# Performance work log

Measured on AMD Instinct MI355X. Metric: run time of the kernel, lower is better.

The kernel has to match this reference:

```python
import jax, jax.numpy as jnp
import numpy as np

B, C, D, TOPK = 4096, 8192, 128, 10


def calc_distmat2(x, y):
    d = (x * x).sum(-1)[:, None] + (y * y).sum(-1)[None, :] - 2.0 * (x @ y.T)
    return jnp.clip(d, 1e-12, 1e12)


def setup_inputs() -> dict:
    key = jax.random.key(0)
    k1, k2, k3 = jax.random.split(key, 3)
    x = jax.random.normal(k1, (B, D), dtype=jnp.float32)
    labels = jax.random.randint(k2, (B,), 0, C)
    # kaiming_normal_(mode='fan_out') on (C, D): fan_out = C, gain = sqrt(2)
    centers = jax.random.normal(k3, (C, D), dtype=jnp.float32) * np.float32(np.sqrt(2.0 / C))
    return {"x": x, "labels": labels, "centers": centers, "topk": TOPK}


def reference(x, labels, centers, topk):
    num_classes = centers.shape[0]
    distmat = calc_distmat2(x, centers)                      # (B, C)
    lab = labels[:, None]                                    # (B, 1)
    dist_pull = jnp.take_along_axis(distmat, lab, axis=1)[:, 0]  # (B,)
    loss_pull = dist_pull.mean()

    # mode 'exp': per-row masked topk over negatives + log-softmax over [pos, neg_topk]
    logits = -distmat                                        # (B, C)
    pos = jnp.take_along_axis(logits, lab, axis=1)           # (B, 1)
    is_pos = lab == jnp.arange(num_classes)[None, :]         # (B, C)
    neg_logits = jnp.where(is_pos, -jnp.inf, logits)
    neg_topk, _ = jax.lax.top_k(neg_logits, topk)            # (B, topk)
    cat = jnp.concatenate([pos, neg_topk], axis=1)           # (B, 1+topk)
    # -log_softmax at index 0 (the positive) per row, averaged ('ccent')
    loss = (-jax.nn.log_softmax(cat, axis=1)[:, 0]).mean()

    # center-to-center repulsion over strictly-lower-triangular pairs
    cent2cent = calc_distmat2(centers, centers)              # (C, C)
    tri = jnp.tril(jnp.ones((num_classes, num_classes), dtype=bool), -1)
    n_pairs = num_classes * (num_classes - 1) // 2
    loss_dis = -jnp.sum(jnp.where(tri, cent2cent, 0.0)) / jnp.float32(n_pairs)

    return (loss, loss_dis, cent2cent, loss_pull)
```

## Files before the change

kernel.cpp:

```cpp
#include <hip/hip_runtime.h>
#include <hip/hip_bf16.h>
#include <math.h>

#define NB 4096
#define NC 8192
#define ND 128
#define NSPLIT 32
#define CPS (NC / NSPLIT)
#define NTILES (CPS / 16)
#define NEGINF -3.0e38f

#define WS_XN 16
#define WS_CN (WS_XN + NB)
#define WS_POS (WS_CN + NC)
#define WS_PART (WS_POS + NB)
#define WS_XB (WS_PART + NB * NSPLIT * 10)
#define WS_CB (WS_XB + NB * ND / 2)

typedef __attribute__((ext_vector_type(8))) short short8v;
typedef __attribute__((ext_vector_type(4))) float f32x4;

__global__ __launch_bounds__(256) void prep_kernel(
    const float* __restrict__ x, const float* __restrict__ c, float* __restrict__ ws) {
  if (blockIdx.x == 0 && threadIdx.x < 16) ws[threadIdx.x] = 0.0f;
  int wid = threadIdx.x >> 6, lane = threadIdx.x & 63;
  int row = blockIdx.x * 4 + wid;
  const float* src;
  float* ndst;
  ushort* bdst;
  if (row < NB) {
    src = x + (size_t)row * ND;
    ndst = ws + WS_XN + row;
    bdst = (ushort*)(ws + WS_XB) + (size_t)row * ND;
  } else {
    int r = row - NB;
    src = c + (size_t)r * ND;
    ndst = ws + WS_CN + r;
    bdst = (ushort*)(ws + WS_CB) + (size_t)r * ND;
  }
  float2 v = *(const float2*)(src + lane * 2);
  __hip_bfloat16 h0 = __float2bfloat16(v.x);
  __hip_bfloat16 h1 = __float2bfloat16(v.y);
  ushort2 u;
  u.x = *(ushort*)&h0;
  u.y = *(ushort*)&h1;
  *(ushort2*)(bdst + lane * 2) = u;
  float s = fmaf(v.x, v.x, v.y * v.y);
#pragma unroll
  for (int off = 32; off; off >>= 1) s += __shfl_down(s, off, 64);
  if (lane == 0) *ndst = s;
}

#define INS10(arr, val)                          \
  {                                              \
    float _v = (val);                            \
    _Pragma("unroll") for (int _k = 0; _k < 10; ++_k) { \
      float _mx = fmaxf(arr[_k], _v);            \
      _v = fminf(arr[_k], _v);                   \
      arr[_k] = _mx;                             \
    }                                            \
  }

#define SW(a, b) { float _x = fmaxf(a, b); b = fminf(a, b); a = _x; }

#define LOADF(d0, d1, d2, d3, IDX)                                            \
  {                                                                           \
    const ushort* cp_ = cb + (size_t)(cbase + (IDX) * 16 + lo) * ND + hi * 8; \
    d0 = *(const short8v*)(cp_ + 0);                                          \
    d1 = *(const short8v*)(cp_ + 32);                                         \
    d2 = *(const short8v*)(cp_ + 64);                                         \
    d3 = *(const short8v*)(cp_ + 96);                                         \
  }

#define EPILOGUE(TL, ACC, CN4)                                                \
  {                                                                           \
    int cb0_ = cbase + (TL) * 16 + hi * 4;                                    \
    float a0 = -(fminf(fmaxf(xn + (CN4).x - 2.0f * (ACC)[0], 1e-12f), 1e12f));\
    float a1 = -(fminf(fmaxf(xn + (CN4).y - 2.0f * (ACC)[1], 1e-12f), 1e12f));\
    float a2 = -(fminf(fmaxf(xn + (CN4).z - 2.0f * (ACC)[2], 1e-12f), 1e12f));\
    float a3 = -(fminf(fmaxf(xn + (CN4).w - 2.0f * (ACC)[3], 1e-12f), 1e12f));\
    bool l0 = (cb0_ + 0 == lab), l1 = (cb0_ + 1 == lab),                      \
         l2 = (cb0_ + 2 == lab), l3 = (cb0_ + 3 == lab);                      \
    posv = l0 ? a0 : posv; posv = l1 ? a1 : posv;                             \
    posv = l2 ? a2 : posv; posv = l3 ? a3 : posv;                             \
    a0 = l0 ? NEGINF : a0; a1 = l1 ? NEGINF : a1;                             \
    a2 = l2 ? NEGINF : a2; a3 = l3 ? NEGINF : a3;                             \
    SW(a0, a1) SW(a2, a3) SW(a0, a2) SW(a1, a3) SW(a1, a2)                    \
    float n0 = fmaxf(a0, top[0]);                                             \
    float n1 = fmaxf(fmaxf(a1, top[1]), fminf(a0, top[0]));                   \
    float n2 = fmaxf(fmaxf(a2, top[2]),                                       \
                     fmaxf(fminf(a0, top[1]), fminf(a1, top[0])));            \
    float n3 = fmaxf(fmaxf(a3, top[3]),                                       \
                     fmaxf(fmaxf(fminf(a0, top[2]), fminf(a1, top[1])),       \
                           fminf(a2, top[0])));                               \
    float n4 = fmaxf(top[4], fmaxf(fmaxf(fminf(a0, top[3]), fminf(a1, top[2])), \
                                   fmaxf(fminf(a2, top[1]), fminf(a3, top[0])))); \
    float n5 = fmaxf(top[5], fmaxf(fmaxf(fminf(a0, top[4]), fminf(a1, top[3])), \
                                   fmaxf(fminf(a2, top[2]), fminf(a3, top[1])))); \
    float n6 = fmaxf(top[6], fmaxf(fmaxf(fminf(a0, top[5]), fminf(a1, top[4])), \
                                   fmaxf(fminf(a2, top[3]), fminf(a3, top[2])))); \
    float n7 = fmaxf(top[7], fmaxf(fmaxf(fminf(a0, top[6]), fminf(a1, top[5])), \
                                   fmaxf(fminf(a2, top[4]), fminf(a3, top[3])))); \
    float n8 = fmaxf(top[8], fmaxf(fmaxf(fminf(a0, top[7]), fminf(a1, top[6])), \
                                   fmaxf(fminf(a2, top[5]), fminf(a3, top[4])))); \
    float n9 = fmaxf(top[9], fmaxf(fmaxf(fminf(a0, top[8]), fminf(a1, top[7])), \
                                   fmaxf(fminf(a2, top[6]), fminf(a3, top[5])))); \
    top[0] = n0; top[1] = n1; top[2] = n2; top[3] = n3; top[4] = n4;          \
    top[5] = n5; top[6] = n6; top[7] = n7; top[8] = n8; top[9] = n9;          \
  }

__global__ __launch_bounds__(256) void xloss_kernel(
    const int* __restrict__ labels, float* __restrict__ ws) {
  int t = threadIdx.x;
  int w = t >> 6, l = t & 63, lo = l & 15, hi = l >> 4;
  int row = blockIdx.x * 64 + w * 16 + lo;
  int cbase = blockIdx.y * CPS;

  const ushort* xb = (const ushort*)(ws + WS_XB);
  const ushort* cb = (const ushort*)(ws + WS_CB);

  const ushort* xrp = xb + (size_t)row * ND + hi * 8;
  short8v xf0 = *(const short8v*)(xrp + 0);
  short8v xf1 = *(const short8v*)(xrp + 32);
  short8v xf2 = *(const short8v*)(xrp + 64);
  short8v xf3 = *(const short8v*)(xrp + 96);

  float xn = ws[WS_XN + row];
  int lab = labels[row];

  float top[10];
#pragma unroll
  for (int k = 0; k < 10; ++k) top[k] = NEGINF;
  float posv = NEGINF;

  short8v pa0, pa1, pa2, pa3, qa0, qa1, qa2, qa3;
  f32x4 cnP, cnQ;
  LOADF(pa0, pa1, pa2, pa3, 0)
  cnP = *(const f32x4*)(ws + WS_CN + cbase + hi * 4);

  for (int tl = 0; tl < NTILES; tl += 2) {
    LOADF(qa0, qa1, qa2, qa3, tl + 1)
    cnQ = *(const f32x4*)(ws + WS_CN + cbase + (tl + 1) * 16 + hi * 4);

    f32x4 accA = {0.f, 0.f, 0.f, 0.f};
    accA = __builtin_amdgcn_mfma_f32_16x16x32_bf16(pa0, xf0, accA, 0, 0, 0);
    accA = __builtin_amdgcn_mfma_f32_16x16x32_bf16(pa1, xf1, accA, 0, 0, 0);
    accA = __builtin_amdgcn_mfma_f32_16x16x32_bf16(pa2, xf2, accA, 0, 0, 0);
    accA = __builtin_amdgcn_mfma_f32_16x16x32_bf16(pa3, xf3, accA, 0, 0, 0);
    f32x4 cnA = cnP;
    int nidx = (tl + 2 < NTILES) ? tl + 2 : tl;
    LOADF(pa0, pa1, pa2, pa3, nidx)
    cnP = *(const f32x4*)(ws + WS_CN + cbase + nidx * 16 + hi * 4);

    EPILOGUE(tl, accA, cnA)

    f32x4 accB = {0.f, 0.f, 0.f, 0.f};
    accB = __builtin_amdgcn_mfma_f32_16x16x32_bf16(qa0, xf0, accB, 0, 0, 0);
    accB = __builtin_amdgcn_mfma_f32_16x16x32_bf16(qa1, xf1, accB, 0, 0, 0);
    accB = __builtin_amdgcn_mfma_f32_16x16x32_bf16(qa2, xf2, accB, 0, 0, 0);
    accB = __builtin_amdgcn_mfma_f32_16x16x32_bf16(qa3, xf3, accB, 0, 0, 0);
    EPILOGUE(tl + 1, accB, cnQ)
  }

  float oth[10];
#pragma unroll
  for (int m = 16; m <= 32; m <<= 1) {
#pragma unroll
    for (int k = 0; k < 10; ++k) oth[k] = __shfl_xor(top[k], m, 64);
#pragma unroll
    for (int k = 0; k < 10; ++k) INS10(top, oth[k])
  }

  if (posv > -1.0e37f) ws[WS_POS + row] = posv;
  if (hi == 0) {
    float* dst = ws + WS_PART + ((size_t)row * NSPLIT + blockIdx.y) * 10;
#pragma unroll
    for (int k = 0; k < 10; ++k) dst[k] = top[k];
  }
}

__global__ __launch_bounds__(256) void c2c_kernel(
    float* __restrict__ ws, float* __restrict__ outmat) {
  __shared__ float red[4];
  int bi = blockIdx.y, bj = blockIdx.x;
  int t = threadIdx.x;
  int w = t >> 6, l = t & 63, lo = l & 15, hi = l >> 4;
  int wm = w >> 1, wn = w & 1;
  int rowb = bi * 128 + wm * 64;
  int colb = bj * 128 + wn * 64;
  const ushort* cb = (const ushort*)(ws + WS_CB);

  f32x4 acc[4][4];
#pragma unroll
  for (int m = 0; m < 4; ++m)
#pragma unroll
    for (int n = 0; n < 4; ++n) acc[m][n] = (f32x4){0.f, 0.f, 0.f, 0.f};

#pragma unroll
  for (int ks = 0; ks < 4; ++ks) {
    short8v af[4], bf[4];
#pragma unroll
    for (int m = 0; m < 4; ++m)
      af[m] = *(const short8v*)(cb + (size_t)(rowb + m * 16 + lo) * ND + ks * 32 + hi * 8);
#pragma unroll
    for (int n = 0; n < 4; ++n)
      bf[n] = *(const short8v*)(cb + (size_t)(colb + n * 16 + lo) * ND + ks * 32 + hi * 8);
#pragma unroll
    for (int m = 0; m < 4; ++m)
#pragma unroll
      for (int n = 0; n < 4; ++n)
        acc[m][n] = __builtin_amdgcn_mfma_f32_16x16x32_bf16(bf[n], af[m], acc[m][n], 0, 0, 0);
  }

  float cni[4];
#pragma unroll
  for (int m = 0; m < 4; ++m) cni[m] = ws[WS_CN + rowb + m * 16 + lo];
  f32x4 cnj[4];
#pragma unroll
  for (int n = 0; n < 4; ++n)
    cnj[n] = *(const f32x4*)(ws + WS_CN + colb + n * 16 + hi * 4);

  float tsum = 0.0f;
#pragma unroll
  for (int m = 0; m < 4; ++m) {
    int gr = rowb + m * 16 + lo;
    float* orow = outmat + (size_t)gr * NC + colb + hi * 4;
#pragma unroll
    for (int n = 0; n < 4; ++n) {
      f32x4 dd;
#pragma unroll
      for (int rr = 0; rr < 4; ++rr)
        dd[rr] = fminf(fmaxf(cni[m] + cnj[n][rr] - 2.0f * acc[m][n][rr], 1e-12f), 1e12f);
      if (bi > bj) {
        tsum += dd[0] + dd[1] + dd[2] + dd[3];
      } else if (bi == bj) {
        int gc0 = colb + n * 16 + hi * 4;
#pragma unroll
        for (int rr = 0; rr < 4; ++rr) tsum += (gr > gc0 + rr) ? dd[rr] : 0.0f;
      }
      *(f32x4*)(orow + n * 16) = dd;
    }
  }

  if (bi >= bj) {
#pragma unroll
    for (int off = 32; off; off >>= 1) tsum += __shfl_down(tsum, off, 64);
    if (l == 0) red[w] = tsum;
    __syncthreads();
    if (t == 0)
      atomicAdd(ws + 4 + (bi % 12), red[0] + red[1] + red[2] + red[3]);
  }
}

__global__ __launch_bounds__(256) void merge_fin_kernel(float* __restrict__ ws,
                                                        float* __restrict__ out) {
  int row = blockIdx.x * 256 + threadIdx.x;
  const f32x4* part = (const f32x4*)(ws + WS_PART + (size_t)row * NSPLIT * 10);
  float top[10];
#pragma unroll
  for (int k = 0; k < 10; ++k) top[k] = NEGINF;
#pragma unroll
  for (int i = 0; i < NSPLIT * 10 / 4; ++i) {
    f32x4 v = part[i];
    INS10(top, v.x)
    INS10(top, v.y)
    INS10(top, v.z)
    INS10(top, v.w)
  }
  float pos = ws[WS_POS + row];
  float mx = fmaxf(pos, top[0]);
  float ssum = expf(pos - mx);
#pragma unroll
  for (int k = 0; k < 10; ++k) ssum += expf(top[k] - mx);
  float lrow = mx + logf(ssum) - pos;
  float prow = -pos;
#pragma unroll
  for (int off = 32; off; off >>= 1) {
    lrow += __shfl_down(lrow, off, 64);
    prow += __shfl_down(prow, off, 64);
  }
  if ((threadIdx.x & 63) == 0) {
    atomicAdd(ws + 0, lrow);
    atomicAdd(ws + 2, prow);
  }
  __syncthreads();
  if (threadIdx.x == 0) {
    __threadfence();
    unsigned tk = atomicAdd((unsigned int*)(ws + 3), 1u);
    if (tk == 15u) {
      float ls = atomicAdd(ws + 0, 0.0f);
      float ps = atomicAdd(ws + 2, 0.0f);
      float ts = 0.0f;
#pragma unroll
      for (int i = 0; i < 12; ++i) ts += ws[4 + i];
      out[0] = ls / 4096.0f;
      out[1] = -ts / 33550336.0f;
      out[2 + (size_t)NC * NC] = ps / 4096.0f;
    }
  }
}

extern "C" void kernel_launch(void* const* d_in, const int* in_sizes, int n_in,
                              void* d_out, int out_size, void* d_ws, size_t ws_size,
                              hipStream_t stream) {
  const float* x = (const float*)d_in[0];
  const int* labels = (const int*)d_in[1];
  const float* centers = (const float*)d_in[2];
  float* out = (float*)d_out;
  float* ws = (float*)d_ws;

  hipLaunchKernelGGL(prep_kernel, dim3((NB + NC) / 4), dim3(256), 0, stream, x, centers, ws);
  hipLaunchKernelGGL(c2c_kernel, dim3(64, 64), dim3(256), 0, stream, ws, out + 2);
  hipLaunchKernelGGL(xloss_kernel, dim3(64, NSPLIT), dim3(256), 0, stream, labels, ws);
  hipLaunchKernelGGL(merge_fin_kernel, dim3(NB / 256), dim3(256), 0, stream, ws, out);
}
```

Before: 190.6 us.

## Merge c2c and xloss kernels into one launch with heterogeneous blocks

Combines the center-to-center distance kernel and the x-loss top-k kernel into one grid, so the compute-heavy xloss blocks (scheduled first) can run alongside the store-bound c2c blocks instead of serializing. It halves the column splits for xloss (longer per-block loops, fewer partials to merge) and halves the c2c tile width to 128x64 with more blocks, adding a launch bound of 5 waves. This risks higher register pressure and longer tail blocks from the xloss side.

```diff
diff --git a/kernel.cpp b/kernel.cpp
--- a/kernel.cpp
+++ b/kernel.cpp
@@ -5,10 +5,12 @@
 #define NB 4096
 #define NC 8192
 #define ND 128
-#define NSPLIT 32
+#define NSPLIT 16
 #define CPS (NC / NSPLIT)
 #define NTILES (CPS / 16)
 #define NEGINF -3.0e38f
+#define XBLKS 1024
+#define CBLKS 8192
 
 #define WS_XN 16
 #define WS_CN (WS_XN + NB)
@@ -109,146 +111,147 @@
     top[5] = n5; top[6] = n6; top[7] = n7; top[8] = n8; top[9] = n9;          \
   }
 
-__global__ __launch_bounds__(256) void xloss_kernel(
-    const int* __restrict__ labels, float* __restrict__ ws) {
+__global__ __launch_bounds__(256, 5) void mega_kernel(
+    const int* __restrict__ labels, float* __restrict__ ws, float* __restrict__ outmat) {
   int t = threadIdx.x;
   int w = t >> 6, l = t & 63, lo = l & 15, hi = l >> 4;
-  int row = blockIdx.x * 64 + w * 16 + lo;
-  int cbase = blockIdx.y * CPS;
-
-  const ushort* xb = (const ushort*)(ws + WS_XB);
+  int bid = blockIdx.x;
   const ushort* cb = (const ushort*)(ws + WS_CB);
 
-  const ushort* xrp = xb + (size_t)row * ND + hi * 8;
-  short8v xf0 = *(const short8v*)(xrp + 0);
-  short8v xf1 = *(const short8v*)(xrp + 32);
-  short8v xf2 = *(const short8v*)(xrp + 64);
-  short8v xf3 = *(const short8v*)(xrp + 96);
-
-  float xn = ws[WS_XN + row];
-  int lab = labels[row];
-
-  float top[10];
-#pragma unroll
-  for (int k = 0; k < 10; ++k) top[k] = NEGINF;
-  float posv = NEGINF;
-
-  short8v pa0, pa1, pa2, pa3, qa0, qa1, qa2, qa3;
-  f32x4 cnP, cnQ;
-  LOADF(pa0, pa1, pa2, pa3, 0)
-  cnP = *(const f32x4*)(ws + WS_CN + cbase + hi * 4);
-
-  for (int tl = 0; tl < NTILES; tl += 2) {
-    LOADF(qa0, qa1, qa2, qa3, tl + 1)
-    cnQ = *(const f32x4*)(ws + WS_CN + cbase + (tl + 1) * 16 + hi * 4);
-
-    f32x4 accA = {0.f, 0.f, 0.f, 0.f};
-    accA = __builtin_amdgcn_mfma_f32_16x16x32_bf16(pa0, xf0, accA, 0, 0, 0);
-    accA = __builtin_amdgcn_mfma_f32_16x16x32_bf16(pa1, xf1, accA, 0, 0, 0);
-    accA = __builtin_amdgcn_mfma_f32_16x16x32_bf16(pa2, xf2, accA, 0, 0, 0);
-    accA = __builtin_amdgcn_mfma_f32_16x16x32_bf16(pa3, xf3, accA, 0, 0, 0);
-    f32x4 cnA = cnP;
-    int nidx = (tl + 2 < NTILES) ? tl + 2 : tl;
-    LOADF(pa0, pa1, pa2, pa3, nidx)
-    cnP = *(const f32x4*)(ws + WS_CN + cbase + nidx * 16 + hi * 4);
-
-    EPILOGUE(tl, accA, cnA)
-
-    f32x4 accB = {0.f, 0.f, 0.f, 0.f};
-    accB = __builtin_amdgcn_mfma_f32_16x16x32_bf16(qa0, xf0, accB, 0, 0, 0);
-    accB = __builtin_amdgcn_mfma_f32_16x16x32_bf16(qa1, xf1, accB, 0, 0, 0);
-    accB = __builtin_amdgcn_mfma_f32_16x16x32_bf16(qa2, xf2, accB, 0, 0, 0);
-    accB = __builtin_amdgcn_mfma_f32_16x16x32_bf16(qa3, xf3, accB, 0, 0, 0);
-    EPILOGUE(tl + 1, accB, cnQ)
-  }
-
-  float oth[10];
-#pragma unroll
-  for (int m = 16; m <= 32; m <<= 1) {
-#pragma unroll
-    for (int k = 0; k < 10; ++k) oth[k] = __shfl_xor(top[k], m, 64);
-#pragma unroll
-    for (int k = 0; k < 10; ++k) INS10(top, oth[k])
-  }
-
-  if (posv > -1.0e37f) ws[WS_POS + row] = posv;
-  if (hi == 0) {
-    float* dst = ws + WS_PART + ((size_t)row * NSPLIT + blockIdx.y) * 10;
-#pragma unroll
-    for (int k = 0; k < 10; ++k) dst[k] = top[k];
-  }
-}
-
-__global__ __launch_bounds__(256) void c2c_kernel(
-    float* __restrict__ ws, float* __restrict__ outmat) {
-  __shared__ float red[4];
-  int bi = blockIdx.y, bj = blockIdx.x;
-  int t = threadIdx.x;
-  int w = t >> 6, l = t & 63, lo = l & 15, hi = l >> 4;
-  int wm = w >> 1, wn = w & 1;
-  int rowb = bi * 128 + wm * 64;
-  int colb = bj * 128 + wn * 64;
-  const ushort* cb = (const ushort*)(ws + WS_CB);
-
-  f32x4 acc[4][4];
-#pragma unroll
-  for (int m = 0; m < 4; ++m)
-#pragma unroll
-    for (int n = 0; n < 4; ++n) acc[m][n] = (f32x4){0.f, 0.f, 0.f, 0.f};
-
-#pragma unroll
-  for (int ks = 0; ks < 4; ++ks) {
-    short8v af[4], bf[4];
+  if (bid < XBLKS) {
+    int bx = bid & 63, by = bid >> 6;
+    int row = bx * 64 + w * 16 + lo;
+    int cbase = by * CPS;
+    const ushort* xb = (const ushort*)(ws + WS_XB);
+
+    const ushort* xrp = xb + (size_t)row * ND + hi * 8;
+    short8v xf0 = *(const short8v*)(xrp + 0);
+    short8v xf1 = *(const short8v*)(xrp + 32);
+    short8v xf2 = *(const short8v*)(xrp + 64);
+    short8v xf3 = *(const short8v*)(xrp + 96);
+
+    float xn = ws[WS_XN + row];
+    int lab = labels[row];
+
+    float top[10];
+#pragma unroll
+    for (int k = 0; k < 10; ++k) top[k] = NEGINF;
+    float posv = NEGINF;
+
+    short8v pa0, pa1, pa2, pa3, qa0, qa1, qa2, qa3;
+    f32x4 cnP, cnQ;
+    LOADF(pa0, pa1, pa2, pa3, 0)
+    cnP = *(const f32x4*)(ws + WS_CN + cbase + hi * 4);
+
+    for (int tl = 0; tl < NTILES; tl += 2) {
+      LOADF(qa0, qa1, qa2, qa3, tl + 1)
+      cnQ = *(const f32x4*)(ws + WS_CN + cbase + (tl + 1) * 16 + hi * 4);
+
+      f32x4 accA = {0.f, 0.f, 0.f, 0.f};
+      accA = __builtin_amdgcn_mfma_f32_16x16x32_bf16(pa0, xf0, accA, 0, 0, 0);
+      accA = __builtin_amdgcn_mfma_f32_16x16x32_bf16(pa1, xf1, accA, 0, 0, 0);
+      accA = __builtin_amdgcn_mfma_f32_16x16x32_bf16(pa2, xf2, accA, 0, 0, 0);
+      accA = __builtin_amdgcn_mfma_f32_16x16x32_bf16(pa3, xf3, accA, 0, 0, 0);
+      f32x4 cnA = cnP;
+      int nidx = (tl + 2 < NTILES) ? tl + 2 : tl;
+      LOADF(pa0, pa1, pa2, pa3, nidx)
+      cnP = *(const f32x4*)(ws + WS_CN + cbase + nidx * 16 + hi * 4);
+
+      EPILOGUE(tl, accA, cnA)
+
+      f32x4 accB = {0.f, 0.f, 0.f, 0.f};
+      accB = __builtin_amdgcn_mfma_f32_16x16x32_bf16(qa0, xf0, accB, 0, 0, 0);
+      accB = __builtin_amdgcn_mfma_f32_16x16x32_bf16(qa1, xf1, accB, 0, 0, 0);
+      accB = __builtin_amdgcn_mfma_f32_16x16x32_bf16(qa2, xf2, accB, 0, 0, 0);
+      accB = __builtin_amdgcn_mfma_f32_16x16x32_bf16(qa3, xf3, accB, 0, 0, 0);
+      EPILOGUE(tl + 1, accB, cnQ)
+    }
+
+    float oth[10];
+#pragma unroll
+    for (int m = 16; m <= 32; m <<= 1) {
+#pragma unroll
+      for (int k = 0; k < 10; ++k) oth[k] = __shfl_xor(top[k], m, 64);
+#pragma unroll
+      for (int k = 0; k < 10; ++k) INS10(top, oth[k])
+    }
+
+    if (posv > -1.0e37f) ws[WS_POS + row] = posv;
+    if (hi == 0) {
+      float* dst = ws + WS_PART + ((size_t)row * NSPLIT + by) * 10;
+#pragma unroll
+      for (int k = 0; k < 10; ++k) dst[k] = top[k];
+    }
+  } else {
+    __shared__ float red[4];
+    int cid = bid - XBLKS;
+    int bi = cid >> 7, bj = cid & 127;
+    int wm = w >> 1, wn = w & 1;
+    int rowb = bi * 128 + wm * 64;
+    int colb = bj * 64 + wn * 32;
+
+    f32x4 acc[4][2];
 #pragma unroll
     for (int m = 0; m < 4; ++m)
-      af[m] = *(const short8v*)(cb + (size_t)(rowb + m * 16 + lo) * ND + ks * 32 + hi * 8);
-#pragma unroll
-    for (int n = 0; n < 4; ++n)
-      bf[n] = *(const short8v*)(cb + (size_t)(colb + n * 16 + lo) * ND + ks * 32 + hi * 8);
-#pragma unroll
-    for (int m = 0; m < 4; ++m)
-#pragma unroll
-      for (int n = 0; n < 4; ++n)
-        acc[m][n] = __builtin_amdgcn_mfma_f32_16x16x32_bf16(bf[n], af[m], acc[m][n], 0, 0, 0);
-  }
-
-  float cni[4];
-#pragma unroll
-  for (int m = 0; m < 4; ++m) cni[m] = ws[WS_CN + rowb + m * 16 + lo];
-  f32x4 cnj[4];
-#pragma unroll
-  for (int n = 0; n < 4; ++n)
-    cnj[n] = *(const f32x4*)(ws + WS_CN + colb + n * 16 + hi * 4);
-
-  float tsum = 0.0f;
-#pragma unroll
-  for (int m = 0; m < 4; ++m) {
-    int gr = rowb + m * 16 + lo;
-    float* orow = outmat + (size_t)gr * NC + colb + hi * 4;
-#pragma unroll
-    for (int n = 0; n < 4; ++n) {
-      f32x4 dd;
-#pragma unroll
-      for (int rr = 0; rr < 4; ++rr)
-        dd[rr] = fminf(fmaxf(cni[m] + cnj[n][rr] - 2.0f * acc[m][n][rr], 1e-12f), 1e12f);
-      if (bi > bj) {
-        tsum += dd[0] + dd[1] + dd[2] + dd[3];
-      } else if (bi == bj) {
-        int gc0 = colb + n * 16 + hi * 4;
-#pragma unroll
-        for (int rr = 0; rr < 4; ++rr) tsum += (gr > gc0 + rr) ? dd[rr] : 0.0f;
+#pragma unroll
+      for (int n = 0; n < 2; ++n) acc[m][n] = (f32x4){0.f, 0.f, 0.f, 0.f};
+
+#pragma unroll
+    for (int ks = 0; ks < 4; ++ks) {
+      short8v af[4], bf[2];
+#pragma unroll
+      for (int m = 0; m < 4; ++m)
+        af[m] = *(const short8v*)(cb + (size_t)(rowb + m * 16 + lo) * ND + ks * 32 + hi * 8);
+#pragma unroll
+      for (int n = 0; n < 2; ++n)
+        bf[n] = *(const short8v*)(cb + (size_t)(colb + n * 16 + lo) * ND + ks * 32 + hi * 8);
+#pragma unroll
+      for (int m = 0; m < 4; ++m)
+#pragma unroll
+        for (int n = 0; n < 2; ++n)
+          acc[m][n] = __builtin_amdgcn_mfma_f32_16x16x32_bf16(bf[n], af[m], acc[m][n], 0, 0, 0);
+    }
+
+    float cni[4];
+#pragma unroll
+    for (int m = 0; m < 4; ++m) cni[m] = ws[WS_CN + rowb + m * 16 + lo];
+    f32x4 cnj[2];
+#pragma unroll
+    for (int n = 0; n < 2; ++n)
+      cnj[n] = *(const f32x4*)(ws + WS_CN + colb + n * 16 + hi * 4);
+
+    bool fullLower = (bj < 2 * bi);
+    bool fullUpper = (bj >= 2 * bi + 2);
+    float tsum = 0.0f;
+#pragma unroll
+    for (int m = 0; m < 4; ++m) {
+      int gr = rowb + m * 16 + lo;
+      float* orow = outmat + (size_t)gr * NC + colb + hi * 4;
+#pragma unroll
+      for (int n = 0; n < 2; ++n) {
+        f32x4 dd;
+#pragma unroll
+        for (int rr = 0; rr < 4; ++rr)
+          dd[rr] = fminf(fmaxf(cni[m] + cnj[n][rr] - 2.0f * acc[m][n][rr], 1e-12f), 1e12f);
+        if (fullLower) {
+          tsum += dd[0] + dd[1] + dd[2] + dd[3];
+        } else if (!fullUpper) {
+          int gc0 = colb + n * 16 + hi * 4;
+#pragma unroll
+          for (int rr = 0; rr < 4; ++rr) tsum += (gr > gc0 + rr) ? dd[rr] : 0.0f;
+        }
+        *(f32x4*)(orow + n * 16) = dd;
       }
-      *(f32x4*)(orow + n * 16) = dd;
-    }
-  }
-
-  if (bi >= bj) {
-#pragma unroll
-    for (int off = 32; off; off >>= 1) tsum += __shfl_down(tsum, off, 64);
-    if (l == 0) red[w] = tsum;
-    __syncthreads();
-    if (t == 0)
-      atomicAdd(ws + 4 + (bi % 12), red[0] + red[1] + red[2] + red[3]);
+    }
+
+    if (!fullUpper) {
+#pragma unroll
+      for (int off = 32; off; off >>= 1) tsum += __shfl_down(tsum, off, 64);
+      if (l == 0) red[w] = tsum;
+      __syncthreads();
+      if (t == 0)
+        atomicAdd(ws + 4 + (bi % 12), red[0] + red[1] + red[2] + red[3]);
+    }
   }
 }
 
@@ -310,7 +313,6 @@
   float* ws = (float*)d_ws;
 
   hipLaunchKernelGGL(prep_kernel, dim3((NB + NC) / 4), dim3(256), 0, stream, x, centers, ws);
-  hipLaunchKernelGGL(c2c_kernel, dim3(64, 64), dim3(256), 0, stream, ws, out + 2);
-  hipLaunchKernelGGL(xloss_kernel, dim3(64, NSPLIT), dim3(256), 0, stream, labels, ws);
+  hipLaunchKernelGGL(mega_kernel, dim3(XBLKS + CBLKS), dim3(256), 0, stream, labels, ws, out + 2);
   hipLaunchKernelGGL(merge_fin_kernel, dim3(NB / 256), dim3(256), 0, stream, ws, out);
 }
```

New measurement: 206.1 us. 8.1% more time.

## Restructure c2c to row-strip streaming and split top-k chains in xloss

Applied to the files above, without the earlier changes.

The c2c kernel changes from 128x128 block tiles with a 4x4 MFMA grid to 16-row strips. Each block holds its A fragment in registers and streams column tiles with double-buffered loads, writing rows contiguously and applying the triangle mask per element. The xloss kernel halves NSPLIT and keeps two independent top-10 lists, and it splits each tile's MFMA accumulation into two chains to shorten dependency chains and raise ILP. This adds register pressure. The strip layout also reloads B tiles from L2 and loses the 2D reuse of the old tiling.

```diff
diff --git a/kernel.cpp b/kernel.cpp
--- a/kernel.cpp
+++ b/kernel.cpp
@@ -5,7 +5,7 @@
 #define NB 4096
 #define NC 8192
 #define ND 128
-#define NSPLIT 32
+#define NSPLIT 16
 #define CPS (NC / NSPLIT)
 #define NTILES (CPS / 16)
 #define NEGINF -3.0e38f
@@ -72,7 +72,7 @@
     d3 = *(const short8v*)(cp_ + 96);                                         \
   }
 
-#define EPILOGUE(TL, ACC, CN4)                                                \
+#define EPILOGUE(TL, ACC, CN4, TOP)                                           \
   {                                                                           \
     int cb0_ = cbase + (TL) * 16 + hi * 4;                                    \
     float a0 = -(fminf(fmaxf(xn + (CN4).x - 2.0f * (ACC)[0], 1e-12f), 1e12f));\
@@ -86,27 +86,27 @@
     a0 = l0 ? NEGINF : a0; a1 = l1 ? NEGINF : a1;                             \
     a2 = l2 ? NEGINF : a2; a3 = l3 ? NEGINF : a3;                             \
     SW(a0, a1) SW(a2, a3) SW(a0, a2) SW(a1, a3) SW(a1, a2)                    \
-    float n0 = fmaxf(a0, top[0]);                                             \
-    float n1 = fmaxf(fmaxf(a1, top[1]), fminf(a0, top[0]));                   \
-    float n2 = fmaxf(fmaxf(a2, top[2]),                                       \
-                     fmaxf(fminf(a0, top[1]), fminf(a1, top[0])));            \
-    float n3 = fmaxf(fmaxf(a3, top[3]),                                       \
-                     fmaxf(fmaxf(fminf(a0, top[2]), fminf(a1, top[1])),       \
-                           fminf(a2, top[0])));                               \
-    float n4 = fmaxf(top[4], fmaxf(fmaxf(fminf(a0, top[3]), fminf(a1, top[2])), \
-                                   fmaxf(fminf(a2, top[1]), fminf(a3, top[0])))); \
-    float n5 = fmaxf(top[5], fmaxf(fmaxf(fminf(a0, top[4]), fminf(a1, top[3])), \
-                                   fmaxf(fminf(a2, top[2]), fminf(a3, top[1])))); \
-    float n6 = fmaxf(top[6], fmaxf(fmaxf(fminf(a0, top[5]), fminf(a1, top[4])), \
-                                   fmaxf(fminf(a2, top[3]), fminf(a3, top[2])))); \
-    float n7 = fmaxf(top[7], fmaxf(fmaxf(fminf(a0, top[6]), fminf(a1, top[5])), \
-                                   fmaxf(fminf(a2, top[4]), fminf(a3, top[3])))); \
-    float n8 = fmaxf(top[8], fmaxf(fmaxf(fminf(a0, top[7]), fminf(a1, top[6])), \
-                                   fmaxf(fminf(a2, top[5]), fminf(a3, top[4])))); \
-    float n9 = fmaxf(top[9], fmaxf(fmaxf(fminf(a0, top[8]), fminf(a1, top[7])), \
-                                   fmaxf(fminf(a2, top[6]), fminf(a3, top[5])))); \
-    top[0] = n0; top[1] = n1; top[2] = n2; top[3] = n3; top[4] = n4;          \
-    top[5] = n5; top[6] = n6; top[7] = n7; top[8] = n8; top[9] = n9;          \
+    float n0 = fmaxf(a0, TOP[0]);                                             \
+    float n1 = fmaxf(fmaxf(a1, TOP[1]), fminf(a0, TOP[0]));                   \
+    float n2 = fmaxf(fmaxf(a2, TOP[2]),                                       \
+                     fmaxf(fminf(a0, TOP[1]), fminf(a1, TOP[0])));            \
+    float n3 = fmaxf(fmaxf(a3, TOP[3]),                                       \
+                     fmaxf(fmaxf(fminf(a0, TOP[2]), fminf(a1, TOP[1])),       \
+                           fminf(a2, TOP[0])));                               \
+    float n4 = fmaxf(TOP[4], fmaxf(fmaxf(fminf(a0, TOP[3]), fminf(a1, TOP[2])), \
+                                   fmaxf(fminf(a2, TOP[1]), fminf(a3, TOP[0])))); \
+    float n5 = fmaxf(TOP[5], fmaxf(fmaxf(fminf(a0, TOP[4]), fminf(a1, TOP[3])), \
+                                   fmaxf(fminf(a2, TOP[2]), fminf(a3, TOP[1])))); \
+    float n6 = fmaxf(TOP[6], fmaxf(fmaxf(fminf(a0, TOP[5]), fminf(a1, TOP[4])), \
+                                   fmaxf(fminf(a2, TOP[3]), fminf(a3, TOP[2])))); \
+    float n7 = fmaxf(TOP[7], fmaxf(fmaxf(fminf(a0, TOP[6]), fminf(a1, TOP[5])), \
+                                   fmaxf(fminf(a2, TOP[4]), fminf(a3, TOP[3])))); \
+    float n8 = fmaxf(TOP[8], fmaxf(fmaxf(fminf(a0, TOP[7]), fminf(a1, TOP[6])), \
+                                   fmaxf(fminf(a2, TOP[5]), fminf(a3, TOP[4])))); \
+    float n9 = fmaxf(TOP[9], fmaxf(fmaxf(fminf(a0, TOP[8]), fminf(a1, TOP[7])), \
+                                   fmaxf(fminf(a2, TOP[6]), fminf(a3, TOP[5])))); \
+    TOP[0] = n0; TOP[1] = n1; TOP[2] = n2; TOP[3] = n3; TOP[4] = n4;          \
+    TOP[5] = n5; TOP[6] = n6; TOP[7] = n7; TOP[8] = n8; TOP[9] = n9;          \
   }
 
 __global__ __launch_bounds__(256) void xloss_kernel(
@@ -128,9 +128,9 @@
   float xn = ws[WS_XN + row];
   int lab = labels[row];
 
-  float top[10];
-#pragma unroll
-  for (int k = 0; k < 10; ++k) top[k] = NEGINF;
+  float topA[10], topB[10];
+#pragma unroll
+  for (int k = 0; k < 10; ++k) { topA[k] = NEGINF; topB[k] = NEGINF; }
   float posv = NEGINF;
 
   short8v pa0, pa1, pa2, pa3, qa0, qa1, qa2, qa3;
@@ -142,114 +142,132 @@
     LOADF(qa0, qa1, qa2, qa3, tl + 1)
     cnQ = *(const f32x4*)(ws + WS_CN + cbase + (tl + 1) * 16 + hi * 4);
 
-    f32x4 accA = {0.f, 0.f, 0.f, 0.f};
-    accA = __builtin_amdgcn_mfma_f32_16x16x32_bf16(pa0, xf0, accA, 0, 0, 0);
-    accA = __builtin_amdgcn_mfma_f32_16x16x32_bf16(pa1, xf1, accA, 0, 0, 0);
-    accA = __builtin_amdgcn_mfma_f32_16x16x32_bf16(pa2, xf2, accA, 0, 0, 0);
-    accA = __builtin_amdgcn_mfma_f32_16x16x32_bf16(pa3, xf3, accA, 0, 0, 0);
+    f32x4 aA1 = {0.f, 0.f, 0.f, 0.f}, aA2 = {0.f, 0.f, 0.f, 0.f};
+    aA1 = __builtin_amdgcn_mfma_f32_16x16x32_bf16(pa0, xf0, aA1, 0, 0, 0);
+    aA1 = __builtin_amdgcn_mfma_f32_16x16x32_bf16(pa1, xf1, aA1, 0, 0, 0);
+    aA2 = __builtin_amdgcn_mfma_f32_16x16x32_bf16(pa2, xf2, aA2, 0, 0, 0);
+    aA2 = __builtin_amdgcn_mfma_f32_16x16x32_bf16(pa3, xf3, aA2, 0, 0, 0);
+    f32x4 accA = aA1 + aA2;
     f32x4 cnA = cnP;
     int nidx = (tl + 2 < NTILES) ? tl + 2 : tl;
     LOADF(pa0, pa1, pa2, pa3, nidx)
     cnP = *(const f32x4*)(ws + WS_CN + cbase + nidx * 16 + hi * 4);
 
-    EPILOGUE(tl, accA, cnA)
-
-    f32x4 accB = {0.f, 0.f, 0.f, 0.f};
-    accB = __builtin_amdgcn_mfma_f32_16x16x32_bf16(qa0, xf0, accB, 0, 0, 0);
-    accB = __builtin_amdgcn_mfma_f32_16x16x32_bf16(qa1, xf1, accB, 0, 0, 0);
-    accB = __builtin_amdgcn_mfma_f32_16x16x32_bf16(qa2, xf2, accB, 0, 0, 0);
-    accB = __builtin_amdgcn_mfma_f32_16x16x32_bf16(qa3, xf3, accB, 0, 0, 0);
-    EPILOGUE(tl + 1, accB, cnQ)
-  }
+    f32x4 aB1 = {0.f, 0.f, 0.f, 0.f}, aB2 = {0.f, 0.f, 0.f, 0.f};
+    aB1 = __builtin_amdgcn_mfma_f32_16x16x32_bf16(qa0, xf0, aB1, 0, 0, 0);
+    aB1 = __builtin_amdgcn_mfma_f32_16x16x32_bf16(qa1, xf1, aB1, 0, 0, 0);
+    aB2 = __builtin_amdgcn_mfma_f32_16x16x32_bf16(qa2, xf2, aB2, 0, 0, 0);
+    aB2 = __builtin_amdgcn_mfma_f32_16x16x32_bf16(qa3, xf3, aB2, 0, 0, 0);
+    f32x4 accB = aB1 + aB2;
+
+    EPILOGUE(tl, accA, cnA, topA)
+    EPILOGUE(tl + 1, accB, cnQ, topB)
+  }
+
+#pragma unroll
+  for (int k = 0; k < 10; ++k) INS10(topA, topB[k])
 
   float oth[10];
 #pragma unroll
   for (int m = 16; m <= 32; m <<= 1) {
 #pragma unroll
-    for (int k = 0; k < 10; ++k) oth[k] = __shfl_xor(top[k], m, 64);
-#pragma unroll
-    for (int k = 0; k < 10; ++k) INS10(top, oth[k])
+    for (int k = 0; k < 10; ++k) oth[k] = __shfl_xor(topA[k], m, 64);
+#pragma unroll
+    for (int k = 0; k < 10; ++k) INS10(topA, oth[k])
   }
 
   if (posv > -1.0e37f) ws[WS_POS + row] = posv;
   if (hi == 0) {
     float* dst = ws + WS_PART + ((size_t)row * NSPLIT + blockIdx.y) * 10;
 #pragma unroll
-    for (int k = 0; k < 10; ++k) dst[k] = top[k];
-  }
-}
+    for (int k = 0; k < 10; ++k) dst[k] = topA[k];
+  }
+}
+
+#define LOADB(d0, d1, d2, d3, GT)                                             \
+  {                                                                           \
+    const ushort* bp_ = cb + (size_t)((GT) * 16 + lo) * ND + hi * 8;          \
+    d0 = *(const short8v*)(bp_ + 0);                                          \
+    d1 = *(const short8v*)(bp_ + 32);                                         \
+    d2 = *(const short8v*)(bp_ + 64);                                         \
+    d3 = *(const short8v*)(bp_ + 96);                                         \
+  }
+
+#define C2CTILE(B0, B1, B2, B3, GT)                                           \
+  {                                                                           \
+    f32x4 c1_ = {0.f, 0.f, 0.f, 0.f}, c2_ = {0.f, 0.f, 0.f, 0.f};            \
+    c1_ = __builtin_amdgcn_mfma_f32_16x16x32_bf16(B0, af0, c1_, 0, 0, 0);     \
+    c1_ = __builtin_amdgcn_mfma_f32_16x16x32_bf16(B1, af1, c1_, 0, 0, 0);     \
+    c2_ = __builtin_amdgcn_mfma_f32_16x16x32_bf16(B2, af2, c2_, 0, 0, 0);     \
+    c2_ = __builtin_amdgcn_mfma_f32_16x16x32_bf16(B3, af3, c2_, 0, 0, 0);     \
+    f32x4 ac_ = c1_ + c2_;                                                    \
+    int gc0_ = (GT) * 16 + hi * 4;                                            \
+    f32x4 cnj_ = *(const f32x4*)(ws + WS_CN + gc0_);                          \
+    f32x4 dd_;                                                                \
+    dd_[0] = fminf(fmaxf(cni + cnj_[0] - 2.0f * ac_[0], 1e-12f), 1e12f);      \
+    dd_[1] = fminf(fmaxf(cni + cnj_[1] - 2.0f * ac_[1], 1e-12f), 1e12f);      \
+    dd_[2] = fminf(fmaxf(cni + cnj_[2] - 2.0f * ac_[2], 1e-12f), 1e12f);      \
+    dd_[3] = fminf(fmaxf(cni + cnj_[3] - 2.0f * ac_[3], 1e-12f), 1e12f);      \
+    if (gc0_ + 3 < gr) {                                                      \
+      tsum += dd_[0] + dd_[1] + dd_[2] + dd_[3];                              \
+    } else if (gc0_ < gr) {                                                   \
+      tsum += (gc0_ + 0 < gr) ? dd_[0] : 0.0f;                                \
+      tsum += (gc0_ + 1 < gr) ? dd_[1] : 0.0f;                                \
+      tsum += (gc0_ + 2 < gr) ? dd_[2] : 0.0f;                                \
+      tsum += (gc0_ + 3 < gr) ? dd_[3] : 0.0f;                                \
+    }                                                                         \
+    *(f32x4*)(orow + gc0_) = dd_;                                             \
+  }
 
 __global__ __launch_bounds__(256) void c2c_kernel(
     float* __restrict__ ws, float* __restrict__ outmat) {
   __shared__ float red[4];
-  int bi = blockIdx.y, bj = blockIdx.x;
   int t = threadIdx.x;
   int w = t >> 6, l = t & 63, lo = l & 15, hi = l >> 4;
-  int wm = w >> 1, wn = w & 1;
-  int rowb = bi * 128 + wm * 64;
-  int colb = bj * 128 + wn * 64;
+  int rb = blockIdx.x * 16;
+  int wt0 = w * 128;
   const ushort* cb = (const ushort*)(ws + WS_CB);
 
-  f32x4 acc[4][4];
-#pragma unroll
-  for (int m = 0; m < 4; ++m)
-#pragma unroll
-    for (int n = 0; n < 4; ++n) acc[m][n] = (f32x4){0.f, 0.f, 0.f, 0.f};
-
-#pragma unroll
-  for (int ks = 0; ks < 4; ++ks) {
-    short8v af[4], bf[4];
-#pragma unroll
-    for (int m = 0; m < 4; ++m)
-      af[m] = *(const short8v*)(cb + (size_t)(rowb + m * 16 + lo) * ND + ks * 32 + hi * 8);
-#pragma unroll
-    for (int n = 0; n < 4; ++n)
-      bf[n] = *(const short8v*)(cb + (size_t)(colb + n * 16 + lo) * ND + ks * 32 + hi * 8);
-#pragma unroll
-    for (int m = 0; m < 4; ++m)
-#pragma unroll
-      for (int n = 0; n < 4; ++n)
-        acc[m][n] = __builtin_amdgcn_mfma_f32_16x16x32_bf16(bf[n], af[m], acc[m][n], 0, 0, 0);
-  }
-
-  float cni[4];
-#pragma unroll
-  for (int m = 0; m < 4; ++m) cni[m] = ws[WS_CN + rowb + m * 16 + lo];
-  f32x4 cnj[4];
-#pragma unroll
-  for (int n = 0; n < 4; ++n)
-    cnj[n] = *(const f32x4*)(ws + WS_CN + colb + n * 16 + hi * 4);
-
+  const ushort* ap = cb + (size_t)(rb + lo) * ND + hi * 8;
+  short8v af0 = *(const short8v*)(ap + 0);
+  short8v af1 = *(const short8v*)(ap + 32);
+  short8v af2 = *(const short8v*)(ap + 64);
+  short8v af3 = *(const short8v*)(ap + 96);
+
+  int gr = rb + lo;
+  float cni = ws[WS_CN + gr];
+  float* orow = outmat + (size_t)gr * NC;
   float tsum = 0.0f;
-#pragma unroll
-  for (int m = 0; m < 4; ++m) {
-    int gr = rowb + m * 16 + lo;
-    float* orow = outmat + (size_t)gr * NC + colb + hi * 4;
-#pragma unroll
-    for (int n = 0; n < 4; ++n) {
-      f32x4 dd;
-#pragma unroll
-      for (int rr = 0; rr < 4; ++rr)
-        dd[rr] = fminf(fmaxf(cni[m] + cnj[n][rr] - 2.0f * acc[m][n][rr], 1e-12f), 1e12f);
-      if (bi > bj) {
-        tsum += dd[0] + dd[1] + dd[2] + dd[3];
-      } else if (bi == bj) {
-        int gc0 = colb + n * 16 + hi * 4;
-#pragma unroll
-        for (int rr = 0; rr < 4; ++rr) tsum += (gr > gc0 + rr) ? dd[rr] : 0.0f;
-      }
-      *(f32x4*)(orow + n * 16) = dd;
-    }
-  }
-
-  if (bi >= bj) {
-#pragma unroll
-    for (int off = 32; off; off >>= 1) tsum += __shfl_down(tsum, off, 64);
-    if (l == 0) red[w] = tsum;
-    __syncthreads();
-    if (t == 0)
-      atomicAdd(ws + 4 + (bi % 12), red[0] + red[1] + red[2] + red[3]);
-  }
+
+  short8v p00, p01, p02, p03, p10, p11, p12, p13;
+  short8v q00, q01, q02, q03, q10, q11, q12, q13;
+  LOADB(p00, p01, p02, p03, wt0 + 0)
+  LOADB(p10, p11, p12, p13, wt0 + 1)
+
+  for (int ck = 0; ck < 64; ck += 2) {
+    int gtQ = wt0 + (ck + 1) * 2;
+    LOADB(q00, q01, q02, q03, gtQ + 0)
+    LOADB(q10, q11, q12, q13, gtQ + 1)
+
+    int gtP = wt0 + ck * 2;
+    C2CTILE(p00, p01, p02, p03, gtP + 0)
+    C2CTILE(p10, p11, p12, p13, gtP + 1)
+
+    int nck = (ck + 2 < 64) ? ck + 2 : ck;
+    int gtN = wt0 + nck * 2;
+    LOADB(p00, p01, p02, p03, gtN + 0)
+    LOADB(p10, p11, p12, p13, gtN + 1)
+
+    C2CTILE(q00, q01, q02, q03, gtQ + 0)
+    C2CTILE(q10, q11, q12, q13, gtQ + 1)
+  }
+
+#pragma unroll
+  for (int off = 32; off; off >>= 1) tsum += __shfl_down(tsum, off, 64);
+  if (l == 0) red[w] = tsum;
+  __syncthreads();
+  if (t == 0)
+    atomicAdd(ws + 4 + (blockIdx.x % 12), red[0] + red[1] + red[2] + red[3]);
 }
 
 __global__ __launch_bounds__(256) void merge_fin_kernel(float* __restrict__ ws,
@@ -310,7 +328,7 @@
   float* ws = (float*)d_ws;
 
   hipLaunchKernelGGL(prep_kernel, dim3((NB + NC) / 4), dim3(256), 0, stream, x, centers, ws);
-  hipLaunchKernelGGL(c2c_kernel, dim3(64, 64), dim3(256), 0, stream, ws, out + 2);
+  hipLaunchKernelGGL(c2c_kernel, dim3(512), dim3(256), 0, stream, ws, out + 2);
   hipLaunchKernelGGL(xloss_kernel, dim3(64, NSPLIT), dim3(256), 0, stream, labels, ws);
   hipLaunchKernelGGL(merge_fin_kernel, dim3(NB / 256), dim3(256), 0, stream, ws, out);
 }
```

After: 266.9 us. 40.0% more time.
